# Kernel optimization log

Measured on AMD Instinct MI355X. Metric: run time of the kernel, lower is better.

The kernel has to match this reference:

```python
import jax, jax.numpy as jnp
import numpy as np

DIM = 768
HEADS = 12
HEAD_DIM = DIM // HEADS  # 64
THETA = 10000.0
B, S = 2, 2048


def rotate_half(x):
    # pairs-interleaved rotate: (x1, x2) -> (-x2, x1)
    xp = x.reshape(x.shape[:-1] + (-1, 2))
    x1, x2 = xp[..., 0], xp[..., 1]
    return jnp.stack((-x2, x1), axis=-1).reshape(x.shape)


def rope_freqs(seq_len, head_dim, dtype):
    inv = 1.0 / (THETA ** (jnp.arange(0, head_dim, 2, dtype=jnp.float32) / head_dim))
    pos = jnp.arange(seq_len, dtype=jnp.float32)
    f = pos[:, None] * inv[None, :]              # [S, head_dim//2]
    f = jnp.repeat(f, 2, axis=-1)                # [S, head_dim]
    return f.astype(dtype)


def apply_rotary(freqs, t):
    # freqs [S, D] broadcasts against t [B, H, S, D]
    return t * jnp.cos(freqs) + rotate_half(t) * jnp.sin(freqs)


def setup_inputs() -> dict:
    key = jax.random.key(0)
    k1, k2, k3 = jax.random.split(key, 3)
    x = jax.random.normal(k1, (B, S, DIM), dtype=jnp.float32)
    W_qkv = jax.random.normal(k2, (3 * DIM, DIM), dtype=jnp.float32) * 0.02
    W_proj = jax.random.normal(k3, (DIM, DIM), dtype=jnp.float32) * 0.02
    b_proj = jnp.zeros((DIM,), dtype=jnp.float32)
    return {"x": x, "W_qkv": W_qkv, "W_proj": W_proj, "b_proj": b_proj}


def reference(x, W_qkv, W_proj, b_proj):
    Bb, Ss, C = x.shape
    qkv = jnp.einsum('bsc,oc->bso', x, W_qkv)                    # [B,S,3C]
    qkv = qkv.reshape(Bb, Ss, 3, HEADS, HEAD_DIM)
    qkv = jnp.transpose(qkv, (2, 0, 3, 1, 4))                    # [3,B,H,S,D]
    q, k, v = qkv[0], qkv[1], qkv[2]
    freqs = rope_freqs(Ss, HEAD_DIM, x.dtype)
    q = apply_rotary(freqs, q)
    k = apply_rotary(freqs, k)
    scale = HEAD_DIM ** -0.5
    scores = jnp.einsum('bhqd,bhkd->bhqk', q, k) * scale         # [B,H,S,S]
    probs = jax.nn.softmax(scores, axis=-1)
    out = jnp.einsum('bhqk,bhkd->bhqd', probs, v)                # [B,H,S,D]
    out = jnp.transpose(out, (0, 2, 1, 3)).reshape(Bb, Ss, C)
    return jnp.einsum('bsc,oc->bso', out, W_proj) + b_proj
```

## Files before the change

kernel.cpp:

```cpp
#include <hip/hip_runtime.h>
#include <math.h>

#define Bq 2
#define Sq 2048
#define Cq 768
#define Hq 12
#define Dq 64

#define PANEL_SHORTS 98304
#define PANELS_X  32
#define PANELS_WQ 18
#define PANELS_WP 6

#define NROWS 49152
#define OPQTR 3145728
#define SPLIT_BLOCKS 2688
#define SM_SHIFT 8.0f

typedef _Float16 f16x8 __attribute__((ext_vector_type(8)));
typedef __fp16 fp16v2 __attribute__((ext_vector_type(2)));
typedef float f32x4 __attribute__((ext_vector_type(4)));
typedef float f32x16 __attribute__((ext_vector_type(16)));
#define MFMA16F(a, b, c) __builtin_amdgcn_mfma_f32_16x16x32_f16(a, b, c, 0, 0, 0)
#define MFMA32F(a, b, c) __builtin_amdgcn_mfma_f32_32x32x16_f16(a, b, c, 0, 0, 0)

#define SCALEQ 0.18033688011112042f

static __device__ inline unsigned short f16bits(float x) {
    _Float16 h = (_Float16)x;
    return __builtin_bit_cast(unsigned short, h);
}
static __device__ inline unsigned int pk16(float a, float b) {
    fp16v2 h = __builtin_amdgcn_cvt_pkrtz(a, b);
    return __builtin_bit_cast(unsigned int, h);
}

static __device__ inline void gld_lds16(const unsigned short* g, unsigned short* l) {
    __builtin_amdgcn_global_load_lds(
        (const __attribute__((address_space(1))) unsigned int*)g,
        (__attribute__((address_space(3))) unsigned int*)l, 16, 0, 0);
}

__global__ __launch_bounds__(256) void split_kernel(
    const float* __restrict__ x, const float* __restrict__ wq,
    const float* __restrict__ wp,
    unsigned short* __restrict__ xs, unsigned short* __restrict__ wqs,
    unsigned short* __restrict__ wps,
    float* __restrict__ ctab, float* __restrict__ stab)
{
    if (blockIdx.x >= SPLIT_BLOCKS) {
        int idx = (blockIdx.x - SPLIT_BLOCKS) * 256 + threadIdx.x;
        int s = idx >> 5;
        int i = idx & 31;
        double f = (double)s * exp(-(double)i * 0.28782313662425573);
        ctab[idx] = (float)cos(f);
        stab[idx] = (float)sin(f);
        return;
    }
    const int cid  = blockIdx.x * 256 + threadIdx.x;
    const int panel = cid / 12288;
    const int pos8  = cid % 12288;
    const int step = pos8 >> 10;
    const int rem  = pos8 & 1023;
    const int J    = rem >> 6;
    const int lane = rem & 63;
    const int rowp = J * 8 + (lane >> 3);
    const int lc   = (lane & 7) ^ (rowp & 7);
    const int k    = step * 64 + lc * 8;
    const float* src; unsigned short* dst; int prow;
    if (panel < PANELS_X) {
        src = x;  dst = xs;  prow = panel;
    } else if (panel < PANELS_X + PANELS_WQ) {
        src = wq; dst = wqs; prow = panel - PANELS_X;
    } else {
        src = wp; dst = wps; prow = panel - PANELS_X - PANELS_WQ;
    }
    const int row = prow * 128 + rowp;
    float4 v0 = *(const float4*)(src + (size_t)row * Cq + k);
    float4 v1 = *(const float4*)(src + (size_t)row * Cq + k + 4);
    unsigned short o[8] = { f16bits(v0.x), f16bits(v0.y), f16bits(v0.z),
                            f16bits(v0.w), f16bits(v1.x), f16bits(v1.y),
                            f16bits(v1.z), f16bits(v1.w) };
    *(uint4*)&dst[(size_t)prow * PANEL_SHORTS + (size_t)pos8 * 8] = *(uint4*)o;
}

template <int MODE, int BM, int BN>
__global__ __launch_bounds__(256) void gemm_mfma_kernel(
    const unsigned short* __restrict__ Apr, const unsigned short* __restrict__ Bpr,
    const float* __restrict__ ctab, const float* __restrict__ stab,
    unsigned short* __restrict__ qp, unsigned short* __restrict__ kp,
    unsigned short* __restrict__ vp,
    float* __restrict__ out0, const float* __restrict__ bias)
{
    constexpr int MI  = BM / 32;
    constexpr int NI  = BN / 32;
    constexpr int WTM = BM / 2;
    constexpr int WTN = BN / 2;
    constexpr int BCH = BN / 8;
    constexpr int ACH = BM / 8;
    constexpr int CPW = (ACH + BCH) / 4;

    __shared__ unsigned short sA[BM * 64];
    __shared__ unsigned short sB[BN * 64];

    const int t    = threadIdx.x;
    const int w    = t >> 6;
    const int lane = t & 63;
    const int ml   = lane & 15;
    const int quad = lane >> 4;
    const int wm   = w >> 1;
    const int wn   = w & 1;

    const int mBase = blockIdx.y * BM;
    const int nBase = blockIdx.x * BN;

    const unsigned short* gpanA = Apr + (size_t)(mBase >> 7) * PANEL_SHORTS;
    const unsigned short* gpanB = Bpr + (size_t)(nBase >> 7) * PANEL_SHORTS;
    const int JbA = (mBase & 127) >> 3;
    const int JbB = (nBase & 127) >> 3;

    f32x4 acc[MI][NI];
    #pragma unroll
    for (int mi = 0; mi < MI; ++mi)
        #pragma unroll
        for (int ni = 0; ni < NI; ++ni)
            acc[mi][ni] = (f32x4){0.f, 0.f, 0.f, 0.f};

    for (int k0 = 0; k0 < 12; ++k0) {
        __syncthreads();
        #pragma unroll
        for (int cc = 0; cc < CPW; ++cc) {
            const int c = w * CPW + cc;
            if (c < BCH) {
                gld_lds16(gpanB + k0 * 8192 + (JbB + c) * 512 + lane * 8,
                          sB + c * 512);
            } else {
                const int a = c - BCH;
                gld_lds16(gpanA + k0 * 8192 + (JbA + a) * 512 + lane * 8,
                          sA + a * 512);
            }
        }
        __syncthreads();

        f16x8 aF[MI][2], bF[NI][2];
        #pragma unroll
        for (int mi = 0; mi < MI; ++mi) {
            const int row = wm * WTM + mi * 16 + ml;
            #pragma unroll
            for (int ks = 0; ks < 2; ++ks)
                aF[mi][ks] = *(const f16x8*)
                    &sA[row * 64 + (((ks * 4 + quad) ^ (row & 7)) << 3)];
        }
        #pragma unroll
        for (int ni = 0; ni < NI; ++ni) {
            const int row = wn * WTN + ni * 16 + ml;
            #pragma unroll
            for (int ks = 0; ks < 2; ++ks)
                bF[ni][ks] = *(const f16x8*)
                    &sB[row * 64 + (((ks * 4 + quad) ^ (row & 7)) << 3)];
        }
        #pragma unroll
        for (int mi = 0; mi < MI; ++mi)
            #pragma unroll
            for (int ni = 0; ni < NI; ++ni) {
                acc[mi][ni] = MFMA16F(aF[mi][0], bF[ni][0], acc[mi][ni]);
                acc[mi][ni] = MFMA16F(aF[mi][1], bF[ni][1], acc[mi][ni]);
            }
    }

    if (MODE == 0) {
        const int which = nBase / Cq;
        #pragma unroll
        for (int mi = 0; mi < MI; ++mi) {
            const int gm = mBase + wm * WTM + mi * 16 + quad * 4;
            const int bb = gm >> 11;
            const int s0 = gm & 2047;
            #pragma unroll
            for (int ni = 0; ni < NI; ++ni) {
                const int gn = nBase + wn * WTN + ni * 16 + ml;
                const int c  = gn - which * Cq;
                const int hh = c >> 6;
                const int dd = c & 63;
                const size_t hb = (size_t)(bb * Hq + hh);
                if (which < 2) {
                    #pragma unroll
                    for (int r = 0; r < 4; ++r) {
                        float val = acc[mi][ni][r];
                        float pv  = __shfl_xor(val, 1, 64);
                        const int fi = (s0 + r) * 32 + (dd >> 1);
                        float c0 = ctab[fi], sn = stab[fi];
                        float o = (dd & 1) ? (val * c0 + pv * sn)
                                           : (val * c0 - pv * sn);
                        if (which == 0) {
                            o *= SCALEQ;
                            qp[(hb * Sq + s0 + r) * 64 + dd] = f16bits(o);
                        } else {
                            const int ss = s0 + r, rr = ss & 63, kt2 = ss >> 6;
                            kp[(hb * 32 + kt2) * 4096 + rr * 64
                               + (((dd >> 3) ^ (rr & 7)) << 3) + (dd & 7)] = f16bits(o);
                        }
                    }
                } else {
                    unsigned short hv[4];
                    #pragma unroll
                    for (int r = 0; r < 4; ++r)
                        hv[r] = f16bits(acc[mi][ni][r]);
                    const int kt2 = s0 >> 6;
                    *(ushort4*)&vp[(hb * 32 + kt2) * 4096 + dd * 64
                        + ((((s0 & 63) >> 3) ^ (dd & 7)) << 3) + (s0 & 7)]
                        = *(ushort4*)hv;
                }
            }
        }
    } else {
        #pragma unroll
        for (int mi = 0; mi < MI; ++mi) {
            const int gm = mBase + wm * WTM + mi * 16 + quad * 4;
            #pragma unroll
            for (int ni = 0; ni < NI; ++ni) {
                const int gn = nBase + wn * WTN + ni * 16 + ml;
                const float bz = bias[gn];
                #pragma unroll
                for (int r = 0; r < 4; ++r)
                    out0[(size_t)(gm + r) * Cq + gn] = acc[mi][ni][r] + bz;
            }
        }
    }
}

__global__ __launch_bounds__(256, 4) void attn_mfma_kernel(
    const unsigned short* __restrict__ qp, const unsigned short* __restrict__ kp,
    const unsigned short* __restrict__ vp, unsigned short* __restrict__ op,
    float* __restrict__ lp)
{
    __shared__ __align__(16) unsigned short smem[16384];
    unsigned short* k_s = smem;
    unsigned short* v_s = smem + 4096;
    unsigned short* pb  = smem + 8192;

    const int t    = threadIdx.x;
    const int w    = t >> 6;
    const int lane = t & 63;
    const int l31  = lane & 31;
    const int hi   = lane >> 5;
    const int bi   = blockIdx.x;
    const int bh   = bi % 24;
    const int rest = bi / 24;
    const int qt   = rest >> 2;
    const int qtr  = rest & 3;

    const bool isV = (w >= 2);
    const unsigned short* gsrc = isV ? vp : kp;
    const int Jb = (w & 1) * 4;
    const size_t gb = (size_t)bh * 131072;
    unsigned short* sdst = isV ? v_s : k_s;

    const size_t qrow = ((size_t)bh * Sq + qt * 128 + w * 32 + l31) * 64;
    f16x8 bQ[4];
    #pragma unroll
    for (int ks = 0; ks < 4; ++ks)
        bQ[ks] = *(const f16x8*)(qp + qrow + ks * 16 + hi * 8);

    float l_st = 0.f;
    f32x16 O0, O1;
    #pragma unroll
    for (int e = 0; e < 16; ++e) { O0[e] = 0.f; O1[e] = 0.f; }

    unsigned short* pbl = pb + (w * 32 + l31) * 64;
    const int qsw = l31 & 7;

    for (int kt8 = 0; kt8 < 8; ++kt8) {
        const int kt = qtr * 8 + kt8;
        __syncthreads();
        {
            const unsigned short* gt = gsrc + gb + (size_t)kt * 4096;
            #pragma unroll
            for (int j = 0; j < 4; ++j)
                gld_lds16(gt + (Jb + j) * 512 + lane * 8, sdst + (Jb + j) * 512);
        }
        __syncthreads();

        f32x16 S0, S1;
        #pragma unroll
        for (int e = 0; e < 16; ++e) { S0[e] = -SM_SHIFT; S1[e] = -SM_SHIFT; }
        #pragma unroll
        for (int ks = 0; ks < 4; ++ks) {
            const int g = ks * 2 + hi;
            {
                const int row = l31;
                f16x8 aK = *(const f16x8*)
                    &k_s[row * 64 + ((g ^ (row & 7)) << 3)];
                S0 = MFMA32F(aK, bQ[ks], S0);
            }
            {
                const int row = 32 + l31;
                f16x8 aK = *(const f16x8*)
                    &k_s[row * 64 + ((g ^ (row & 7)) << 3)];
                S1 = MFMA32F(aK, bQ[ks], S1);
            }
        }

        #pragma unroll
        for (int kt2 = 0; kt2 < 2; ++kt2) {
            #pragma unroll
            for (int g = 0; g < 4; ++g) {
                float p0, p1, p2, p3;
                if (kt2 == 0) {
                    p0 = exp2f(S0[g * 4 + 0]); p1 = exp2f(S0[g * 4 + 1]);
                    p2 = exp2f(S0[g * 4 + 2]); p3 = exp2f(S0[g * 4 + 3]);
                } else {
                    p0 = exp2f(S1[g * 4 + 0]); p1 = exp2f(S1[g * 4 + 1]);
                    p2 = exp2f(S1[g * 4 + 2]); p3 = exp2f(S1[g * 4 + 3]);
                }
                l_st += (p0 + p1) + (p2 + p3);
                uint2 u;
                u.x = pk16(p0, p1);
                u.y = pk16(p2, p3);
                const int gran = kt2 * 4 + g;
                *(uint2*)&pbl[((gran ^ qsw) << 3) + hi * 4] = u;
            }
        }

        #pragma unroll
        for (int kstep = 0; kstep < 4; ++kstep) {
            const int gran = kstep * 2 + hi;
            uint4 pu = *(const uint4*)&pbl[((gran ^ qsw) << 3)];
            f16x8 bP = __builtin_bit_cast(f16x8, pu);
            {
                const int row = l31;
                f16x8 aV = *(const f16x8*)
                    &v_s[row * 64 + ((gran ^ (row & 7)) << 3)];
                O0 = MFMA32F(aV, bP, O0);
            }
            {
                const int row = 32 + l31;
                f16x8 aV = *(const f16x8*)
                    &v_s[row * 64 + ((gran ^ (row & 7)) << 3)];
                O1 = MFMA32F(aV, bP, O1);
            }
        }
    }

    l_st += __shfl_xor(l_st, 32, 64);

    const int srow = qt * 128 + w * 32 + l31;
    const size_t rowb = (size_t)qtr * NROWS + (size_t)bh * 2048 + srow;
    if (lane < 32) lp[rowb] = l_st;
    const float il = 1.0f / l_st;
    #pragma unroll
    for (int dt2 = 0; dt2 < 2; ++dt2) {
        #pragma unroll
        for (int g = 0; g < 4; ++g) {
            unsigned short o4[4];
            #pragma unroll
            for (int r = 0; r < 4; ++r) {
                float ov = dt2 ? O1[g * 4 + r] : O0[g * 4 + r];
                o4[r] = f16bits(ov * il);
            }
            *(ushort4*)&op[rowb * 64 + dt2 * 32 + g * 8 + hi * 4] = *(ushort4*)o4;
        }
    }
}

__global__ __launch_bounds__(256) void combine_kernel(
    const unsigned short* __restrict__ op, const float* __restrict__ lp,
    unsigned short* __restrict__ attns)
{
    const int g   = blockIdx.x * 256 + threadIdx.x;
    const int row = g >> 3;
    const int ch  = g & 7;
    const int bh  = row >> 11;
    const int s   = row & 2047;

    const float w0 = lp[row];
    const float w1 = lp[NROWS + row];
    const float w2 = lp[2 * NROWS + row];
    const float w3 = lp[3 * NROWS + row];
    const float inv = 1.0f / (((w0 + w1) + (w2 + w3)));

    f16x8 h0 = *(const f16x8*)(op + (size_t)row * 64 + ch * 8);
    f16x8 h1 = *(const f16x8*)(op + (size_t)OPQTR + (size_t)row * 64 + ch * 8);
    f16x8 h2 = *(const f16x8*)(op + (size_t)2 * OPQTR + (size_t)row * 64 + ch * 8);
    f16x8 h3 = *(const f16x8*)(op + (size_t)3 * OPQTR + (size_t)row * 64 + ch * 8);
    unsigned short o[8];
    #pragma unroll
    for (int j = 0; j < 8; ++j) {
        float v = (w0 * (float)h0[j] + w1 * (float)h1[j])
                + (w2 * (float)h2[j] + w3 * (float)h3[j]);
        o[j] = f16bits(v * inv);
    }

    const int bb = bh / Hq, hh = bh % Hq;
    const int mrow = bb * 2048 + s;
    const int panel = mrow >> 7, r128 = mrow & 127;
    const size_t addr = (size_t)panel * PANEL_SHORTS
                      + (r128 >> 3) * 512 + (r128 & 7) * 64
                      + (size_t)hh * 8192
                      + ((ch ^ (r128 & 7)) << 3);
    *(uint4*)&attns[addr] = *(uint4*)o;
}

extern "C" void kernel_launch(void* const* d_in, const int* in_sizes, int n_in,
                              void* d_out, int out_size, void* d_ws, size_t ws_size,
                              hipStream_t stream) {
    const float* x     = (const float*)d_in[0];
    const float* Wqkv  = (const float*)d_in[1];
    const float* Wproj = (const float*)d_in[2];
    const float* bproj = (const float*)d_in[3];
    float* out = (float*)d_out;

    char* p = (char*)d_ws;
    unsigned short* xs    = (unsigned short*)p; p += (size_t)PANELS_X  * PANEL_SHORTS * 2;
    unsigned short* wqs   = (unsigned short*)p; p += (size_t)PANELS_WQ * PANEL_SHORTS * 2;
    unsigned short* wps   = (unsigned short*)p; p += (size_t)PANELS_WP * PANEL_SHORTS * 2;
    unsigned short* qp    = (unsigned short*)p; p += (size_t)24 * Sq * 64 * 2;
    unsigned short* kp    = (unsigned short*)p; p += (size_t)24 * 131072 * 2;
    unsigned short* vp    = (unsigned short*)p; p += (size_t)24 * 131072 * 2;
    unsigned short* attns = (unsigned short*)p; p += (size_t)PANELS_X * PANEL_SHORTS * 2;
    unsigned short* op    = (unsigned short*)p; p += (size_t)4 * OPQTR * 2;
    float* lp             = (float*)p;          p += (size_t)4 * NROWS * 4;
    float* ctab = (float*)p; p += (size_t)Sq * 32 * 4;
    float* stab = (float*)p; p += (size_t)Sq * 32 * 4;

    split_kernel<<<SPLIT_BLOCKS + 256, 256, 0, stream>>>(
        x, Wqkv, Wproj, xs, wqs, wps, ctab, stab);
    gemm_mfma_kernel<0, 64, 128><<<dim3(18, 64), 256, 0, stream>>>(
        xs, wqs, ctab, stab, qp, kp, vp, nullptr, nullptr);
    attn_mfma_kernel<<<dim3(24 * 64), 256, 0, stream>>>(qp, kp, vp, op, lp);
    combine_kernel<<<dim3(1536), 256, 0, stream>>>(op, lp, attns);
    gemm_mfma_kernel<1, 64, 64><<<dim3(12, 64), 256, 0, stream>>>(
        attns, wps, ctab, stab, nullptr, nullptr, nullptr, out, bproj);
}
```

Before: 172.3 us.

## Fuse split-KV combine into attention via per-tile atomic counters

Removes the separate combine kernel. Each attention block now bumps a per-(head, query tile) counter after writing its partial output, and the last of the four key-quarter blocks merges the partials and writes the fp16 panel layout. The counters are zeroed by two extra blocks in the split kernel. This saves a kernel launch and lets the combine overlap with attention blocks still running, at the cost of a threadfence, an atomic per block, and serialized combine work in the last-finishing blocks.

Measured after the change: 435.0 us. +152.4%, slower.

```diff
diff --git a/kernel.cpp b/kernel.cpp
--- a/kernel.cpp
+++ b/kernel.cpp
@@ -15,6 +15,7 @@
 #define NROWS 49152
 #define OPQTR 3145728
 #define SPLIT_BLOCKS 2688
+#define NGROUPS 384
 #define SM_SHIFT 8.0f
 
 typedef _Float16 f16x8 __attribute__((ext_vector_type(8)));
@@ -46,8 +47,14 @@
     const float* __restrict__ wp,
     unsigned short* __restrict__ xs, unsigned short* __restrict__ wqs,
     unsigned short* __restrict__ wps,
-    float* __restrict__ ctab, float* __restrict__ stab)
+    float* __restrict__ ctab, float* __restrict__ stab,
+    int* __restrict__ cnt)
 {
+    if (blockIdx.x >= SPLIT_BLOCKS + 256) {
+        const int i = (blockIdx.x - SPLIT_BLOCKS - 256) * 256 + threadIdx.x;
+        if (i < NGROUPS) cnt[i] = 0;
+        return;
+    }
     if (blockIdx.x >= SPLIT_BLOCKS) {
         int idx = (blockIdx.x - SPLIT_BLOCKS) * 256 + threadIdx.x;
         int s = idx >> 5;
@@ -231,9 +238,11 @@
 __global__ __launch_bounds__(256, 4) void attn_mfma_kernel(
     const unsigned short* __restrict__ qp, const unsigned short* __restrict__ kp,
     const unsigned short* __restrict__ vp, unsigned short* __restrict__ op,
-    float* __restrict__ lp)
+    float* __restrict__ lp, int* __restrict__ cnt,
+    unsigned short* __restrict__ attns)
 {
     __shared__ __align__(16) unsigned short smem[16384];
+    __shared__ int sOld;
     unsigned short* k_s = smem;
     unsigned short* v_s = smem + 4096;
     unsigned short* pb  = smem + 8192;
@@ -360,44 +369,43 @@
             *(ushort4*)&op[rowb * 64 + dt2 * 32 + g * 8 + hi * 4] = *(ushort4*)o4;
         }
     }
-}
-
-__global__ __launch_bounds__(256) void combine_kernel(
-    const unsigned short* __restrict__ op, const float* __restrict__ lp,
-    unsigned short* __restrict__ attns)
-{
-    const int g   = blockIdx.x * 256 + threadIdx.x;
-    const int row = g >> 3;
-    const int ch  = g & 7;
-    const int bh  = row >> 11;
-    const int s   = row & 2047;
-
-    const float w0 = lp[row];
-    const float w1 = lp[NROWS + row];
-    const float w2 = lp[2 * NROWS + row];
-    const float w3 = lp[3 * NROWS + row];
-    const float inv = 1.0f / (((w0 + w1) + (w2 + w3)));
-
-    f16x8 h0 = *(const f16x8*)(op + (size_t)row * 64 + ch * 8);
-    f16x8 h1 = *(const f16x8*)(op + (size_t)OPQTR + (size_t)row * 64 + ch * 8);
-    f16x8 h2 = *(const f16x8*)(op + (size_t)2 * OPQTR + (size_t)row * 64 + ch * 8);
-    f16x8 h3 = *(const f16x8*)(op + (size_t)3 * OPQTR + (size_t)row * 64 + ch * 8);
-    unsigned short o[8];
-    #pragma unroll
-    for (int j = 0; j < 8; ++j) {
-        float v = (w0 * (float)h0[j] + w1 * (float)h1[j])
-                + (w2 * (float)h2[j] + w3 * (float)h3[j]);
-        o[j] = f16bits(v * inv);
-    }
-
-    const int bb = bh / Hq, hh = bh % Hq;
-    const int mrow = bb * 2048 + s;
-    const int panel = mrow >> 7, r128 = mrow & 127;
-    const size_t addr = (size_t)panel * PANEL_SHORTS
-                      + (r128 >> 3) * 512 + (r128 & 7) * 64
-                      + (size_t)hh * 8192
-                      + ((ch ^ (r128 & 7)) << 3);
-    *(uint4*)&attns[addr] = *(uint4*)o;
+
+    __threadfence();
+    if (t == 0) sOld = atomicAdd(&cnt[bh * 16 + qt], 1);
+    __syncthreads();
+    if (sOld == 3) {
+        __threadfence();
+        const int bb = bh / Hq, hh = bh % Hq;
+        for (int c = t; c < 1024; c += 256) {
+            const int r  = c >> 3;
+            const int ch = c & 7;
+            const int s  = qt * 128 + r;
+            const size_t row = (size_t)bh * 2048 + s;
+            const float w0 = lp[row];
+            const float w1 = lp[NROWS + row];
+            const float w2 = lp[2 * NROWS + row];
+            const float w3 = lp[3 * NROWS + row];
+            const float inv = 1.0f / ((w0 + w1) + (w2 + w3));
+            f16x8 h0 = *(const f16x8*)(op + row * 64 + ch * 8);
+            f16x8 h1 = *(const f16x8*)(op + (size_t)OPQTR + row * 64 + ch * 8);
+            f16x8 h2 = *(const f16x8*)(op + (size_t)2 * OPQTR + row * 64 + ch * 8);
+            f16x8 h3 = *(const f16x8*)(op + (size_t)3 * OPQTR + row * 64 + ch * 8);
+            unsigned short o[8];
+            #pragma unroll
+            for (int j = 0; j < 8; ++j) {
+                float v = (w0 * (float)h0[j] + w1 * (float)h1[j])
+                        + (w2 * (float)h2[j] + w3 * (float)h3[j]);
+                o[j] = f16bits(v * inv);
+            }
+            const int mrow = bb * 2048 + s;
+            const int panel = mrow >> 7, r128 = mrow & 127;
+            const size_t addr = (size_t)panel * PANEL_SHORTS
+                              + (r128 >> 3) * 512 + (r128 & 7) * 64
+                              + (size_t)hh * 8192
+                              + ((ch ^ (r128 & 7)) << 3);
+            *(uint4*)&attns[addr] = *(uint4*)o;
+        }
+    }
 }
 
 extern "C" void kernel_launch(void* const* d_in, const int* in_sizes, int n_in,
@@ -419,15 +427,16 @@
     unsigned short* attns = (unsigned short*)p; p += (size_t)PANELS_X * PANEL_SHORTS * 2;
     unsigned short* op    = (unsigned short*)p; p += (size_t)4 * OPQTR * 2;
     float* lp             = (float*)p;          p += (size_t)4 * NROWS * 4;
+    int* cnt              = (int*)p;            p += (size_t)NGROUPS * 4;
     float* ctab = (float*)p; p += (size_t)Sq * 32 * 4;
     float* stab = (float*)p; p += (size_t)Sq * 32 * 4;
 
-    split_kernel<<<SPLIT_BLOCKS + 256, 256, 0, stream>>>(
-        x, Wqkv, Wproj, xs, wqs, wps, ctab, stab);
+    split_kernel<<<SPLIT_BLOCKS + 256 + 2, 256, 0, stream>>>(
+        x, Wqkv, Wproj, xs, wqs, wps, ctab, stab, cnt);
     gemm_mfma_kernel<0, 64, 128><<<dim3(18, 64), 256, 0, stream>>>(
         xs, wqs, ctab, stab, qp, kp, vp, nullptr, nullptr);
-    attn_mfma_kernel<<<dim3(24 * 64), 256, 0, stream>>>(qp, kp, vp, op, lp);
-    combine_kernel<<<dim3(1536), 256, 0, stream>>>(op, lp, attns);
+    attn_mfma_kernel<<<dim3(24 * 64), 256, 0, stream>>>(
+        qp, kp, vp, op, lp, cnt, attns);
     gemm_mfma_kernel<1, 64, 64><<<dim3(12, 64), 256, 0, stream>>>(
         attns, wps, ctab, stab, nullptr, nullptr, nullptr, out, bproj);
 }
```
